# Kernel tuning notes

Hardware: AMD Instinct MI355X
Metric: run time of the kernel (lower is better)

## Reference

```python
import jax, jax.numpy as jnp
import numpy as np

MODEL_DIM = 128
N_ATOMS = 2048
ATOM_SIZE = 512
N_SAMPLES = 2 ** 15
FACTOR = 1.0
TAU = 1.0
B, E = 8, 64


def _stack(x, w0, b0, w1, b1, w2, b2):
    # LinearOutputStack(model_dim, 2, out_channels=...): 2 hidden layers + output
    h = jax.nn.leaky_relu(x @ w0 + b0, 0.2)
    h = jax.nn.leaky_relu(h @ w1 + b1, 0.2)
    return h @ w2 + b2


def _fft_shift(a, shift):
    # a: [B, E, n], shift: [B, E, 1] (fractional shift in units of n samples * 0.5)
    n = a.shape[-1]
    shift_samples = shift * n * 0.5  # [B, E, 1]
    a = jnp.pad(a, ((0, 0), (0, 0), (0, n * 2)))
    spec = jnp.fft.rfft(a, axis=-1, norm='ortho')  # [B, E, n_coeffs] complex
    n_coeffs = spec.shape[-1]
    phase = (jnp.arange(n_coeffs) * 2j * jnp.pi) / n_coeffs  # [n_coeffs]
    spec = spec * jnp.exp(-phase[None, None, :] * shift_samples)
    samples = jnp.fft.irfft(spec, axis=-1, norm='ortho')
    return samples[..., :n]


def setup_inputs() -> dict:
    key = jax.random.key(0)
    ks = jax.random.split(key, 24)
    w = lambda k, i, o: (jax.random.normal(k, (i, o), jnp.float32) * 0.1)
    z = lambda o: jnp.zeros((o,), jnp.float32)
    return {
        'x': jax.random.normal(ks[0], (B, E, MODEL_DIM), jnp.float32),
        'times': jax.random.uniform(ks[1], (B, E, 1), jnp.float32),
        'gumbel_u': jax.random.uniform(ks[2], (B, E, N_ATOMS), jnp.float32),
        'atoms': jax.random.uniform(ks[3], (N_ATOMS, ATOM_SIZE), jnp.float32, -1.0, 1.0),
        'tw0': w(ks[4], MODEL_DIM, MODEL_DIM), 'tb0': z(MODEL_DIM),
        'tw1': w(ks[5], MODEL_DIM, MODEL_DIM), 'tb1': z(MODEL_DIM),
        'tw2': w(ks[6], MODEL_DIM, 1), 'tb2': z(1),
        'sw0': w(ks[7], MODEL_DIM, MODEL_DIM), 'sb0': z(MODEL_DIM),
        'sw1': w(ks[8], MODEL_DIM, MODEL_DIM), 'sb1': z(MODEL_DIM),
        'sw2': w(ks[9], MODEL_DIM, N_ATOMS), 'sb2': z(N_ATOMS),
        'aw0': w(ks[10], MODEL_DIM, MODEL_DIM), 'ab0': z(MODEL_DIM),
        'aw1': w(ks[11], MODEL_DIM, MODEL_DIM), 'ab1': z(MODEL_DIM),
        'aw2': w(ks[12], MODEL_DIM, 1), 'ab2': z(1),
    }


def reference(x, times, gumbel_u, atoms,
              tw0, tb0, tw1, tb1, tw2, tb2,
              sw0, sb0, sw1, sb1, sw2, sb2,
              aw0, ab0, aw1, ab1, aw2, ab2):
    time = jax.nn.sigmoid(_stack(x, tw0, tb0, tw1, tb1, tw2, tb2)) * FACTOR + times  # [B,E,1]
    amp = _stack(x, aw0, ab0, aw1, ab1, aw2, ab2) ** 2  # [B,E,1]
    logits = _stack(x, sw0, sb0, sw1, sb1, sw2, sb2)  # [B,E,N_ATOMS]

    # hard gumbel-softmax with straight-through estimator
    eps = 1e-10
    g = -jnp.log(-jnp.log(gumbel_u + eps) + eps)
    y_soft = jax.nn.softmax((logits + g) / TAU, axis=-1)
    y_hard = jax.nn.one_hot(jnp.argmax(y_soft, axis=-1), N_ATOMS, dtype=y_soft.dtype)
    sel = y_hard - jax.lax.stop_gradient(y_soft) + y_soft

    normed = atoms / (jnp.linalg.norm(atoms, axis=-1, keepdims=True) + 1e-8)
    a = (sel @ normed) * amp  # [B,E,ATOM_SIZE]
    a = jnp.pad(a, ((0, 0), (0, 0), (0, N_SAMPLES - ATOM_SIZE)))  # [B,E,N_SAMPLES]
    final = _fft_shift(a, time)
    return jnp.sum(final, axis=1, keepdims=True)  # [B,1,N_SAMPLES]
```

## Files before the change

kernel.cpp:

```cpp
#include <hip/hip_runtime.h>
#include <math.h>

#define MD 128
#define NA 2048
#define AS 512
#define NS 32768
#define NBE 512
#define W1 768
#define W2 1280
#define PI 3.14159265358979323846
#define KTH ((float)(PI / 98304.0))

__device__ __forceinline__ float lrelu(float v) { return v > 0.f ? v : 0.2f * v; }

__device__ __forceinline__ float p8_far(float tf, float4 A, float4 B, float4 C)
{
  float u  = tf - A.x;
  float th = u * KTH;
  float sn = __sinf(th);
  float cs = __cosf(th);
  float c  = cs * __builtin_amdgcn_rcpf(sn);
  float u2  = __builtin_fmaf(c, c, 1.f);
  float c2  = c + c;
  float u22 = u2 + u2;
  float a2  = c * u2;
  float a3  = (-1.f / 3.f) * __builtin_fmaf(c2, a2, u2 * u2);
  float a4  = 0.5f * __builtin_fmaf(-c, a3, u2 * a2);
  float s5  = __builtin_fmaf(c2, a4, a2 * a2);
  s5        = __builtin_fmaf(-u22, a3, s5);
  float a5  = -0.2f * s5;
  float s6  = __builtin_fmaf(c, a5, a2 * a3);
  s6        = __builtin_fmaf(-u2, a4, s6);
  float a6  = (-1.f / 3.f) * s6;
  float s7  = __builtin_fmaf(c2, a6, a3 * a3);
  s7        = __builtin_fmaf(-u22, a5, s7);
  s7        = __builtin_fmaf(2.f * a2, a4, s7);
  float a7  = (-1.f / 7.f) * s7;
  float s8  = __builtin_fmaf(c, a7, a3 * a4);
  s8        = __builtin_fmaf(-u2, a6, s8);
  s8        = __builtin_fmaf(a2, a5, s8);
  float a8  = -0.25f * s8;
  float y = c * A.w;
  y = __builtin_fmaf(-u2, B.x, y);
  y = __builtin_fmaf(a2, B.y, y);
  y = __builtin_fmaf(a3, B.z, y);
  y = __builtin_fmaf(a4, B.w, y);
  y = __builtin_fmaf(a5, C.x, y);
  y = __builtin_fmaf(a6, C.y, y);
  y = __builtin_fmaf(a7, C.z, y);
  y = __builtin_fmaf(a8, C.w, y);
  bool farq = (tf < A.y) || (tf >= A.z);
  return farq ? y : 0.f;
}

__global__ __launch_bounds__(128) void hidden_kernel(
    const float* __restrict__ x, const float* __restrict__ times,
    const float* __restrict__ tw0, const float* __restrict__ tb0,
    const float* __restrict__ tw1, const float* __restrict__ tb1,
    const float* __restrict__ tw2, const float* __restrict__ tb2,
    const float* __restrict__ sw0, const float* __restrict__ sb0,
    const float* __restrict__ sw1, const float* __restrict__ sb1,
    const float* __restrict__ aw0, const float* __restrict__ ab0,
    const float* __restrict__ aw1, const float* __restrict__ ab1,
    const float* __restrict__ aw2, const float* __restrict__ ab2,
    float* __restrict__ timev, float* __restrict__ ampv,
    float* __restrict__ h2sel, float* __restrict__ out)
{
  const int rg = blockIdx.x;
  const int stack = blockIdx.y;
  const int tid = threadIdx.x;

  {
    const int gtid = (stack * 128 + rg) * 128 + tid;
    float4* out4 = (float4*)out;
    const float4 z = make_float4(0.f, 0.f, 0.f, 0.f);
    for (int i = gtid; i < (8 * NS) / 4; i += 49152) out4[i] = z;
  }

  __shared__ float xs[4][MD];
  __shared__ double dA[4][MD], dB[4][MD];
  __shared__ float fA[4][MD], fB[4][MD];

#pragma unroll
  for (int j = 0; j < 4; ++j) xs[j][tid] = x[(rg * 4 + j) * MD + tid];
  __syncthreads();

  if (stack == 0) {
    {
      double b = (double)tb0[tid];
      double s[4] = {b, b, b, b};
#pragma unroll 8
      for (int k = 0; k < MD; ++k) {
        double w = (double)tw0[k * MD + tid];
#pragma unroll
        for (int j = 0; j < 4; ++j) s[j] += (double)xs[j][k] * w;
      }
#pragma unroll
      for (int j = 0; j < 4; ++j) dA[j][tid] = s[j] > 0.0 ? s[j] : 0.2 * s[j];
      __syncthreads();
    }
    {
      double b = (double)tb1[tid];
      double s[4] = {b, b, b, b};
#pragma unroll 8
      for (int k = 0; k < MD; ++k) {
        double w = (double)tw1[k * MD + tid];
#pragma unroll
        for (int j = 0; j < 4; ++j) s[j] += dA[j][k] * w;
      }
#pragma unroll
      for (int j = 0; j < 4; ++j) dB[j][tid] = s[j] > 0.0 ? s[j] : 0.2 * s[j];
      __syncthreads();
    }
    {
      double w2 = (double)tw2[tid];
#pragma unroll
      for (int j = 0; j < 4; ++j) dA[j][tid] = dB[j][tid] * w2;
      __syncthreads();
      for (int off = 64; off > 0; off >>= 1) {
        if (tid < off) {
#pragma unroll
          for (int j = 0; j < 4; ++j) dA[j][tid] += dA[j][tid + off];
        }
        __syncthreads();
      }
      if (tid == 0) {
#pragma unroll
        for (int j = 0; j < 4; ++j) {
          double tval = dA[j][0] + (double)tb2[0];
          double sg = 1.0 / (1.0 + exp(-tval));
          float tf = (float)sg;
          timev[rg * 4 + j] = tf * 1.0f + times[rg * 4 + j];
        }
      }
    }
  } else if (stack == 1) {
    {
      float b = ab0[tid];
      float s[4] = {b, b, b, b};
#pragma unroll 8
      for (int k = 0; k < MD; ++k) {
        float w = aw0[k * MD + tid];
#pragma unroll
        for (int j = 0; j < 4; ++j) s[j] += xs[j][k] * w;
      }
#pragma unroll
      for (int j = 0; j < 4; ++j) fA[j][tid] = lrelu(s[j]);
      __syncthreads();
    }
    {
      float b = ab1[tid];
      float s[4] = {b, b, b, b};
#pragma unroll 8
      for (int k = 0; k < MD; ++k) {
        float w = aw1[k * MD + tid];
#pragma unroll
        for (int j = 0; j < 4; ++j) s[j] += fA[j][k] * w;
      }
#pragma unroll
      for (int j = 0; j < 4; ++j) fB[j][tid] = lrelu(s[j]);
      __syncthreads();
    }
    {
      float w2 = aw2[tid];
#pragma unroll
      for (int j = 0; j < 4; ++j) fA[j][tid] = fB[j][tid] * w2;
      __syncthreads();
      for (int off = 64; off > 0; off >>= 1) {
        if (tid < off) {
#pragma unroll
          for (int j = 0; j < 4; ++j) fA[j][tid] += fA[j][tid + off];
        }
        __syncthreads();
      }
      if (tid == 0) {
#pragma unroll
        for (int j = 0; j < 4; ++j) {
          float av = fA[j][0] + ab2[0];
          ampv[rg * 4 + j] = av * av;
        }
      }
    }
  } else {
    {
      float b = sb0[tid];
      float s[4] = {b, b, b, b};
#pragma unroll 8
      for (int k = 0; k < MD; ++k) {
        float w = sw0[k * MD + tid];
#pragma unroll
        for (int j = 0; j < 4; ++j) s[j] += xs[j][k] * w;
      }
#pragma unroll
      for (int j = 0; j < 4; ++j) fA[j][tid] = lrelu(s[j]);
      __syncthreads();
    }
    {
      float b = sb1[tid];
      float s[4] = {b, b, b, b};
#pragma unroll 8
      for (int k = 0; k < MD; ++k) {
        float w = sw1[k * MD + tid];
#pragma unroll
        for (int j = 0; j < 4; ++j) s[j] += fA[j][k] * w;
      }
#pragma unroll
      for (int j = 0; j < 4; ++j)
        h2sel[(rg * 4 + j) * MD + tid] = lrelu(s[j]);
    }
  }
}

__global__ __launch_bounds__(128) void logits_kernel(
    const float* __restrict__ h2sel, const float* __restrict__ gu,
    const float* __restrict__ sw2, const float* __restrict__ sb2,
    float2* __restrict__ partials)
{
  const int ot = blockIdx.x;
  const int beg = blockIdx.y;
  const int tid = threadIdx.x;
  const int o = ot * 128 + tid;
  const int wave = tid >> 6, lane = tid & 63;

  __shared__ float h2s[4][MD];
  __shared__ float wv[2][4];
  __shared__ int wi[2][4];

#pragma unroll
  for (int j = 0; j < 4; ++j) h2s[j][tid] = h2sel[(beg * 4 + j) * MD + tid];
  __syncthreads();

  float b = sb2[o];
  float acc[4] = {b, b, b, b};
#pragma unroll 16
  for (int k = 0; k < MD; ++k) {
    float w = sw2[k * NA + o];
#pragma unroll
    for (int j = 0; j < 4; ++j) acc[j] = fmaf(h2s[j][k], w, acc[j]);
  }

#pragma unroll
  for (int j = 0; j < 4; ++j) {
    float u = gu[(beg * 4 + j) * NA + o];
    float g = -logf(-logf(u + 1e-10f) + 1e-10f);
    float v = acc[j] + g;
    int idx = o;
    for (int off = 32; off > 0; off >>= 1) {
      float ov = __shfl_xor(v, off);
      int oi = __shfl_xor(idx, off);
      if (ov > v || (ov == v && oi < idx)) { v = ov; idx = oi; }
    }
    if (lane == 0) { wv[wave][j] = v; wi[wave][j] = idx; }
  }
  __syncthreads();
  if (tid == 0) {
#pragma unroll
    for (int j = 0; j < 4; ++j) {
      float v0 = wv[0][j], v1 = wv[1][j];
      int i0 = wi[0][j], i1 = wi[1][j];
      bool take1 = (v1 > v0) || (v1 == v0 && i1 < i0);
      float bv = take1 ? v1 : v0;
      int bi = take1 ? i1 : i0;
      partials[(beg * 4 + j) * 16 + ot] = make_float2(bv, __int_as_float(bi));
    }
  }
}

__global__ __launch_bounds__(128) void finalize_kernel(
    const float2* __restrict__ partials, const float* __restrict__ timev,
    const float* __restrict__ ampv, const float* __restrict__ atoms,
    float* __restrict__ G, int* __restrict__ m0s, float* __restrict__ fracs,
    float4* __restrict__ params, float4* __restrict__ mom2)
{
  const int be = blockIdx.x;
  const int tid = threadIdx.x;
  __shared__ float red[128];
  __shared__ float m_red[128][13];
  __shared__ float sc_coef, sc_inv;
  __shared__ int sc_idx;

  if (tid < 64) {
    float v = -3.4e38f;
    int idx = 0x7fffffff;
    if (tid < 16) {
      float2 p = partials[be * 16 + tid];
      v = p.x;
      idx = __float_as_int(p.y);
    }
    for (int off = 8; off > 0; off >>= 1) {
      float ov = __shfl_xor(v, off);
      int oi = __shfl_xor(idx, off);
      if (ov > v || (ov == v && oi < idx)) { v = ov; idx = oi; }
    }
    if (tid == 0) sc_idx = idx;
  }
  __syncthreads();
  const int idx = sc_idx;

  const float4 a4 = ((const float4*)(atoms + (size_t)idx * AS))[tid];

  {
    float ss = a4.x * a4.x + a4.y * a4.y + a4.z * a4.z + a4.w * a4.w;
    red[tid] = ss;
    __syncthreads();
    for (int off = 64; off > 0; off >>= 1) {
      if (tid < off) red[tid] += red[tid + off];
      __syncthreads();
    }
    if (tid == 0) {
      sc_inv = 1.f / (sqrtf(red[0]) + 1e-8f);
      double Nc = (double)timev[be] * (1610612736.0 / 49153.0);
      double rr = rint(Nc);
      int m0 = (int)rr;
      float fr = (float)(Nc - rr);
      if (fabsf(fr) < 1e-9f) fr = (fr < 0.f) ? -1e-9f : 1e-9f;
      m0s[be] = m0;
      fracs[be] = fr;
      sc_coef = ampv[be] * ((m0 & 1) ? 1.0f : -1.0f) *
                sinf((float)PI * fr) * (1.0f / 98304.0f);
      red[64] = (float)m0;
      red[65] = fr;
    }
    __syncthreads();
  }

  const float cf = sc_coef * sc_inv;
  float mk[13];
#pragma unroll
  for (int k = 0; k < 13; ++k) mk[k] = 0.f;
  const float av4[4] = {a4.x * cf, a4.y * cf, a4.z * cf, a4.w * cf};
  float4 gv4;
  float* gvp = (float*)&gv4;
  const int t0 = tid * 4;
#pragma unroll
  for (int j = 0; j < 4; ++j) {
    const int t = t0 + j;
    float gv = (j & 1) ? -av4[j] : av4[j];
    gvp[j] = gv;
    float q = (255.5f - (float)t) * KTH;
    float pw = gv;
    mk[0] += pw;
#pragma unroll
    for (int k = 1; k < 13; ++k) { pw *= q; mk[k] += pw; }
  }
  ((float4*)(G + (size_t)be * AS))[tid] = gv4;
#pragma unroll
  for (int k = 0; k < 13; ++k) m_red[tid][k] = mk[k];
  __syncthreads();
  for (int off = 64; off > 0; off >>= 1) {
    if (tid < off) {
#pragma unroll
      for (int k = 0; k < 13; ++k) m_red[tid][k] += m_red[tid + off][k];
    }
    __syncthreads();
  }
  if (tid == 0) {
    int m0 = (int)red[64];
    float fr = red[65];
    float uc = (float)((double)m0 + (double)fr + 255.5);
    params[be * 3 + 0] = make_float4(uc, (float)(m0 - W1), (float)(m0 + W2), m_red[0][0]);
    params[be * 3 + 1] = make_float4(m_red[0][1], m_red[0][2], m_red[0][3], m_red[0][4]);
    params[be * 3 + 2] = make_float4(m_red[0][5], m_red[0][6], m_red[0][7], m_red[0][8]);
    mom2[be] = make_float4(m_red[0][9], m_red[0][10], m_red[0][11], m_red[0][12]);
  }
}

__global__ __launch_bounds__(256) void field_kernel(
    const float4* __restrict__ params, const float4* __restrict__ mom2,
    const float* __restrict__ G, const int* __restrict__ m0s,
    const float* __restrict__ fracs, float* __restrict__ out)
{
  __shared__ float4 SMEM[768];
  const int bid = blockIdx.x;
  const int tid = threadIdx.x;

  if (bid >= 512) {
    const int idx2 = bid - 512;
    const int b = idx2 >> 7;
    const int seg = idx2 & 127;
    float* Cf   = (float*)SMEM;
    int*   scnt = (int*)(Cf + 32);
    int*   slst = scnt + 2;

    const int w = tid >> 6;
    const int e = tid & 63;
    if (w < 2) {
      const int tile = 2 * seg + w;
      const int be = b * 64 + e;
      const float4 A  = params[be * 3 + 0];
      const float4 B4 = params[be * 3 + 1];
      const float4 C4 = params[be * 3 + 2];
      const float4 D4 = mom2[be];
      const float M[13] = {A.w, B4.x, B4.y, B4.z, B4.w,
                           C4.x, C4.y, C4.z, C4.w, D4.x, D4.y, D4.z, D4.w};

      const float ts = (float)(tile * 128);
      const float te = ts + 128.f;
      const float lo = A.y, hi = A.z;
      const bool inter   = (lo < te) && (hi > ts);
      const bool inside  = (lo <= ts) && (te <= hi);
      const bool special = inter && !inside;

      float Bj[13];
#pragma unroll
      for (int j = 0; j < 13; ++j) Bj[j] = 0.f;

      if (!inter) {
        const float th = (ts + 63.5f - A.x) * KTH;
        const float sn = __sinf(th), cs = __cosf(th);
        const float c = cs * __builtin_amdgcn_rcpf(sn);
        float a[13];
        a[0] = c; a[1] = -__builtin_fmaf(c, c, 1.f);
        float s;
        s = 2.f * a[0] * a[1];                                      a[2]  = -0.5f * s;
        s = __builtin_fmaf(2.f * a[0], a[2], a[1] * a[1]);          a[3]  = (-1.f / 3.f) * s;
        s = 2.f * (a[0] * a[3] + a[1] * a[2]);                      a[4]  = -0.25f * s;
        s = __builtin_fmaf(2.f, a[0] * a[4] + a[1] * a[3], a[2] * a[2]); a[5] = -0.2f * s;
        s = 2.f * (a[0] * a[5] + a[1] * a[4] + a[2] * a[3]);        a[6]  = (-1.f / 6.f) * s;
        s = __builtin_fmaf(2.f, a[0] * a[6] + a[1] * a[5] + a[2] * a[4], a[3] * a[3]); a[7] = (-1.f / 7.f) * s;
        s = 2.f * (a[0] * a[7] + a[1] * a[6] + a[2] * a[5] + a[3] * a[4]); a[8] = -0.125f * s;
        s = __builtin_fmaf(2.f, a[0] * a[8] + a[1] * a[7] + a[2] * a[6] + a[3] * a[5], a[4] * a[4]); a[9] = (-1.f / 9.f) * s;
        s = 2.f * (a[0] * a[9] + a[1] * a[8] + a[2] * a[7] + a[3] * a[6] + a[4] * a[5]); a[10] = -0.1f * s;
        s = __builtin_fmaf(2.f, a[0] * a[10] + a[1] * a[9] + a[2] * a[8] + a[3] * a[7] + a[4] * a[6], a[5] * a[5]); a[11] = (-1.f / 11.f) * s;
        s = 2.f * (a[0] * a[11] + a[1] * a[10] + a[2] * a[9] + a[3] * a[8] + a[4] * a[7] + a[5] * a[6]); a[12] = (-1.f / 12.f) * s;

        const float BIN[13][13] = {
          {1,0,0,0,0,0,0,0,0,0,0,0,0},
          {1,1,0,0,0,0,0,0,0,0,0,0,0},
          {1,2,1,0,0,0,0,0,0,0,0,0,0},
          {1,3,3,1,0,0,0,0,0,0,0,0,0},
          {1,4,6,4,1,0,0,0,0,0,0,0,0},
          {1,5,10,10,5,1,0,0,0,0,0,0,0},
          {1,6,15,20,15,6,1,0,0,0,0,0,0},
          {1,7,21,35,35,21,7,1,0,0,0,0,0},
          {1,8,28,56,70,56,28,8,1,0,0,0,0},
          {1,9,36,84,126,126,84,36,9,1,0,0,0},
          {1,10,45,120,210,252,210,120,45,10,1,0,0},
          {1,11,55,165,330,462,462,330,165,55,11,1,0},
          {1,12,66,220,495,792,924,792,495,220,66,12,1}};
#pragma unroll
        for (int j = 0; j < 13; ++j) {
          float acc = 0.f;
#pragma unroll
          for (int m = j; m < 13; ++m)
            acc = __builtin_fmaf(BIN[m][j] * a[m], M[m - j], acc);
          Bj[j] = acc;
        }
      }

#pragma unroll
      for (int j = 0; j < 13; ++j) {
#pragma unroll
        for (int off = 32; off > 0; off >>= 1)
          Bj[j] += __shfl_xor(Bj[j], off);
      }
      if (e == 0) {
#pragma unroll
        for (int j = 0; j < 13; ++j) Cf[w * 16 + j] = Bj[j];
      }
      unsigned long long msk = __ballot(special);
      if (special) {
        int pos = __popcll(msk & ((1ull << e) - 1ull));
        slst[w * 64 + pos] = be;
      }
      if (e == 0) scnt[w] = (int)__popcll(msk);
    }
    __syncthreads();

    const int t = seg * 256 + tid;
    const int tw = tid >> 7;
    const float* cc = Cf + tw * 16;
    const float tf = (float)t;
    const float h = (tf - ((float)((2 * seg + tw) * 128) + 63.5f)) * KTH;
    float y = cc[12];
    y = __builtin_fmaf(y, h, cc[11]);
    y = __builtin_fmaf(y, h, cc[10]);
    y = __builtin_fmaf(y, h, cc[9]);
    y = __builtin_fmaf(y, h, cc[8]);
    y = __builtin_fmaf(y, h, cc[7]);
    y = __builtin_fmaf(y, h, cc[6]);
    y = __builtin_fmaf(y, h, cc[5]);
    y = __builtin_fmaf(y, h, cc[4]);
    y = __builtin_fmaf(y, h, cc[3]);
    y = __builtin_fmaf(y, h, cc[2]);
    y = __builtin_fmaf(y, h, cc[1]);
    y = __builtin_fmaf(y, h, cc[0]);

    const int cnt = scnt[tw];
    for (int i = 0; i < cnt; ++i) {
      const int se = slst[tw * 64 + i];
      const float4 A  = params[se * 3 + 0];
      const float4 B4 = params[se * 3 + 1];
      const float4 C4 = params[se * 3 + 2];
      y += p8_far(tf, A, B4, C4);
    }
    atomicAdd(&out[b * NS + t], (t & 1) ? -y : y);
    return;
  }

  const int be = bid;
  const int m0 = m0s[be];
  const int start = m0 - W1;
  if (start >= NS) return;
  const float fr = fracs[be];
  const int b = be >> 6;

  float4* Tsplit = SMEM;
  float*  Tf = (float*)Tsplit;
  float*  Gl = (float*)(SMEM + 640);
  const float4* Gl4 = SMEM + 640;

  for (int i = tid; i < AS; i += 256) Gl[i] = G[be * AS + i];
  for (int i = tid; i < 2560; i += 256) {
    int v = start - 511 + i;
    float w = (float)(v - m0) - fr;
    float th = w * KTH;
    float q = th * th;
    float sn = th * __builtin_fmaf(q, __builtin_fmaf(q, (1.f / 120.f), (-1.f / 6.f)), 1.f);
    float cs = __builtin_fmaf(q, __builtin_fmaf(q, (1.f / 24.f), -0.5f), 1.f);
    float val = cs * __builtin_amdgcn_rcpf(sn);
    int g = i >> 2;
    int s = (g >> 1) * 4 + (i & 3) + (g & 1) * 1280;
    Tf[s] = val;
  }
  __syncthreads();

  float acc[8];
#pragma unroll
  for (int r = 0; r < 8; ++r) acc[r] = 0.f;

  float Wf[16];
  {
    float4 qa = Tsplit[tid];
    float4 qb = Tsplit[320 + tid];
    Wf[0] = qa.x; Wf[1] = qa.y; Wf[2] = qa.z; Wf[3] = qa.w;
    Wf[4] = qb.x; Wf[5] = qb.y; Wf[6] = qb.z; Wf[7] = qb.w;
  }
#pragma unroll 4
  for (int k = 0; k < 64; ++k) {
    float4 qa = Tsplit[tid + k + 1];
    float4 qb = Tsplit[320 + tid + k + 1];
    Wf[8]  = qa.x; Wf[9]  = qa.y; Wf[10] = qa.z; Wf[11] = qa.w;
    Wf[12] = qb.x; Wf[13] = qb.y; Wf[14] = qb.z; Wf[15] = qb.w;
    const int tc = 504 - 8 * k;
    const float4 gq0 = Gl4[tc >> 2];
    const float4 gq1 = Gl4[(tc >> 2) + 1];
    const float gvals[8] = {gq0.x, gq0.y, gq0.z, gq0.w,
                            gq1.x, gq1.y, gq1.z, gq1.w};
#pragma unroll
    for (int d = 0; d < 8; ++d) {
      const float gv = gvals[d];
#pragma unroll
      for (int r = 0; r < 8; ++r)
        acc[r] = fmaf(gv, Wf[7 + r - d], acc[r]);
    }
#pragma unroll
    for (int m = 0; m < 8; ++m) Wf[m] = Wf[m + 8];
  }

  const int tb = start + tid * 8;
#pragma unroll
  for (int r = 0; r < 8; ++r) {
    int t = tb + r;
    if (t >= 0 && t < NS) {
      float v = (t & 1) ? -acc[r] : acc[r];
      atomicAdd(&out[b * NS + t], v);
    }
  }
}

extern "C" void kernel_launch(void* const* d_in, const int* in_sizes, int n_in,
                              void* d_out, int out_size, void* d_ws, size_t ws_size,
                              hipStream_t stream) {
  const float* x     = (const float*)d_in[0];
  const float* times = (const float*)d_in[1];
  const float* gu    = (const float*)d_in[2];
  const float* atoms = (const float*)d_in[3];
  const float* tw0 = (const float*)d_in[4];  const float* tb0 = (const float*)d_in[5];
  const float* tw1 = (const float*)d_in[6];  const float* tb1 = (const float*)d_in[7];
  const float* tw2 = (const float*)d_in[8];  const float* tb2 = (const float*)d_in[9];
  const float* sw0 = (const float*)d_in[10]; const float* sb0 = (const float*)d_in[11];
  const float* sw1 = (const float*)d_in[12]; const float* sb1 = (const float*)d_in[13];
  const float* sw2 = (const float*)d_in[14]; const float* sb2 = (const float*)d_in[15];
  const float* aw0 = (const float*)d_in[16]; const float* ab0 = (const float*)d_in[17];
  const float* aw1 = (const float*)d_in[18]; const float* ab1 = (const float*)d_in[19];
  const float* aw2 = (const float*)d_in[20]; const float* ab2 = (const float*)d_in[21];

  char* wsb = (char*)d_ws;
  float*  G        = (float*)wsb;
  int*    m0s      = (int*)(wsb + 1048576);
  float*  fracs    = (float*)(wsb + 1050624);
  float4* params   = (float4*)(wsb + 1052672);
  float*  timev    = (float*)(wsb + 1077248);
  float*  ampv     = (float*)(wsb + 1079296);
  float4* mom2     = (float4*)(wsb + 1081344);
  float*  h2sel    = (float*)(wsb + 1089536);
  float2* partials = (float2*)(wsb + 1351680);

  hidden_kernel<<<dim3(NBE / 4, 3), 128, 0, stream>>>(
      x, times, tw0, tb0, tw1, tb1, tw2, tb2,
      sw0, sb0, sw1, sb1, aw0, ab0, aw1, ab1, aw2, ab2,
      timev, ampv, h2sel, (float*)d_out);

  logits_kernel<<<dim3(16, NBE / 4), 128, 0, stream>>>(h2sel, gu, sw2, sb2, partials);

  finalize_kernel<<<NBE, 128, 0, stream>>>(partials, timev, ampv, atoms,
                                           G, m0s, fracs, params, mom2);

  field_kernel<<<1536, 256, 0, stream>>>(params, mom2, G, m0s, fracs,
                                         (float*)d_out);
}
```

Measured before the change: 69.27 us.

## Fuse hidden and logits kernels, recomputing selection MLP per output tile

Merges the hidden-layer kernel and the logits/argmax kernel into one launch of 2304 blocks. The first 2048 blocks each recompute the two selection-stack hidden layers for their four rows before computing a 128-wide logits tile and the gumbel argmax, which removes the h2sel round trip and one kernel launch. The remaining blocks compute the time and amp stacks, and the output zeroing is spread one float4 per thread. The cost is recomputing the 128x128 hidden layers 16 times per row group.

Result: slower. 72.60 us (+4.8%).

```diff
diff --git a/kernel.cpp b/kernel.cpp
--- a/kernel.cpp
+++ b/kernel.cpp
@@ -53,33 +53,113 @@
   return farq ? y : 0.f;
 }
 
-__global__ __launch_bounds__(128) void hidden_kernel(
+__global__ __launch_bounds__(128) void prepA_kernel(
     const float* __restrict__ x, const float* __restrict__ times,
+    const float* __restrict__ gu,
     const float* __restrict__ tw0, const float* __restrict__ tb0,
     const float* __restrict__ tw1, const float* __restrict__ tb1,
     const float* __restrict__ tw2, const float* __restrict__ tb2,
     const float* __restrict__ sw0, const float* __restrict__ sb0,
     const float* __restrict__ sw1, const float* __restrict__ sb1,
+    const float* __restrict__ sw2, const float* __restrict__ sb2,
     const float* __restrict__ aw0, const float* __restrict__ ab0,
     const float* __restrict__ aw1, const float* __restrict__ ab1,
     const float* __restrict__ aw2, const float* __restrict__ ab2,
     float* __restrict__ timev, float* __restrict__ ampv,
-    float* __restrict__ h2sel, float* __restrict__ out)
+    float2* __restrict__ partials, float* __restrict__ out)
 {
-  const int rg = blockIdx.x;
-  const int stack = blockIdx.y;
+  const int bid = blockIdx.x;
   const int tid = threadIdx.x;
 
   {
-    const int gtid = (stack * 128 + rg) * 128 + tid;
-    float4* out4 = (float4*)out;
-    const float4 z = make_float4(0.f, 0.f, 0.f, 0.f);
-    for (int i = gtid; i < (8 * NS) / 4; i += 49152) out4[i] = z;
+    const int gtid = bid * 128 + tid;
+    if (gtid < (8 * NS) / 4) {
+      ((float4*)out)[gtid] = make_float4(0.f, 0.f, 0.f, 0.f);
+    }
   }
 
   __shared__ float xs[4][MD];
+  __shared__ float fA[4][MD], fB[4][MD];
+
+  if (bid < 2048) {
+    const int ot  = bid & 15;
+    const int beg = bid >> 4;
+    const int o = ot * 128 + tid;
+    const int wave = tid >> 6, lane = tid & 63;
+    __shared__ float wv[2][4];
+    __shared__ int wi[2][4];
+
+#pragma unroll
+    for (int j = 0; j < 4; ++j) xs[j][tid] = x[(beg * 4 + j) * MD + tid];
+    __syncthreads();
+
+    {
+      float b = sb0[tid];
+      float s[4] = {b, b, b, b};
+#pragma unroll 8
+      for (int k = 0; k < MD; ++k) {
+        float w = sw0[k * MD + tid];
+#pragma unroll
+        for (int j = 0; j < 4; ++j) s[j] += xs[j][k] * w;
+      }
+#pragma unroll
+      for (int j = 0; j < 4; ++j) fA[j][tid] = lrelu(s[j]);
+      __syncthreads();
+    }
+    {
+      float b = sb1[tid];
+      float s[4] = {b, b, b, b};
+#pragma unroll 8
+      for (int k = 0; k < MD; ++k) {
+        float w = sw1[k * MD + tid];
+#pragma unroll
+        for (int j = 0; j < 4; ++j) s[j] += fA[j][k] * w;
+      }
+#pragma unroll
+      for (int j = 0; j < 4; ++j) fB[j][tid] = lrelu(s[j]);
+      __syncthreads();
+    }
+
+    float b = sb2[o];
+    float acc[4] = {b, b, b, b};
+#pragma unroll 16
+    for (int k = 0; k < MD; ++k) {
+      float w = sw2[k * NA + o];
+#pragma unroll
+      for (int j = 0; j < 4; ++j) acc[j] = fmaf(fB[j][k], w, acc[j]);
+    }
+
+#pragma unroll
+    for (int j = 0; j < 4; ++j) {
+      float u = gu[(beg * 4 + j) * NA + o];
+      float g = -logf(-logf(u + 1e-10f) + 1e-10f);
+      float v = acc[j] + g;
+      int idx = o;
+      for (int off = 32; off > 0; off >>= 1) {
+        float ov = __shfl_xor(v, off);
+        int oi = __shfl_xor(idx, off);
+        if (ov > v || (ov == v && oi < idx)) { v = ov; idx = oi; }
+      }
+      if (lane == 0) { wv[wave][j] = v; wi[wave][j] = idx; }
+    }
+    __syncthreads();
+    if (tid == 0) {
+#pragma unroll
+      for (int j = 0; j < 4; ++j) {
+        float v0 = wv[0][j], v1 = wv[1][j];
+        int i0 = wi[0][j], i1 = wi[1][j];
+        bool take1 = (v1 > v0) || (v1 == v0 && i1 < i0);
+        float bv = take1 ? v1 : v0;
+        int bi = take1 ? i1 : i0;
+        partials[(beg * 4 + j) * 16 + ot] = make_float2(bv, __int_as_float(bi));
+      }
+    }
+    return;
+  }
+
   __shared__ double dA[4][MD], dB[4][MD];
-  __shared__ float fA[4][MD], fB[4][MD];
+  const int stack = (bid < 2176) ? 0 : 1;
+  const int rg = bid - (stack == 0 ? 2048 : 2176);
 
 #pragma unroll
   for (int j = 0; j < 4; ++j) xs[j][tid] = x[(rg * 4 + j) * MD + tid];
@@ -134,7 +214,7 @@
         }
       }
     }
-  } else if (stack == 1) {
+  } else {
     {
       float b = ab0[tid];
       float s[4] = {b, b, b, b};
@@ -180,88 +260,6 @@
           ampv[rg * 4 + j] = av * av;
         }
       }
-    }
-  } else {
-    {
-      float b = sb0[tid];
-      float s[4] = {b, b, b, b};
-#pragma unroll 8
-      for (int k = 0; k < MD; ++k) {
-        float w = sw0[k * MD + tid];
-#pragma unroll
-        for (int j = 0; j < 4; ++j) s[j] += xs[j][k] * w;
-      }
-#pragma unroll
-      for (int j = 0; j < 4; ++j) fA[j][tid] = lrelu(s[j]);
-      __syncthreads();
-    }
-    {
-      float b = sb1[tid];
-      float s[4] = {b, b, b, b};
-#pragma unroll 8
-      for (int k = 0; k < MD; ++k) {
-        float w = sw1[k * MD + tid];
-#pragma unroll
-        for (int j = 0; j < 4; ++j) s[j] += fA[j][k] * w;
-      }
-#pragma unroll
-      for (int j = 0; j < 4; ++j)
-        h2sel[(rg * 4 + j) * MD + tid] = lrelu(s[j]);
-    }
-  }
-}
-
-__global__ __launch_bounds__(128) void logits_kernel(
-    const float* __restrict__ h2sel, const float* __restrict__ gu,
-    const float* __restrict__ sw2, const float* __restrict__ sb2,
-    float2* __restrict__ partials)
-{
-  const int ot = blockIdx.x;
-  const int beg = blockIdx.y;
-  const int tid = threadIdx.x;
-  const int o = ot * 128 + tid;
-  const int wave = tid >> 6, lane = tid & 63;
-
-  __shared__ float h2s[4][MD];
-  __shared__ float wv[2][4];
-  __shared__ int wi[2][4];
-
-#pragma unroll
-  for (int j = 0; j < 4; ++j) h2s[j][tid] = h2sel[(beg * 4 + j) * MD + tid];
-  __syncthreads();
-
-  float b = sb2[o];
-  float acc[4] = {b, b, b, b};
-#pragma unroll 16
-  for (int k = 0; k < MD; ++k) {
-    float w = sw2[k * NA + o];
-#pragma unroll
-    for (int j = 0; j < 4; ++j) acc[j] = fmaf(h2s[j][k], w, acc[j]);
-  }
-
-#pragma unroll
-  for (int j = 0; j < 4; ++j) {
-    float u = gu[(beg * 4 + j) * NA + o];
-    float g = -logf(-logf(u + 1e-10f) + 1e-10f);
-    float v = acc[j] + g;
-    int idx = o;
-    for (int off = 32; off > 0; off >>= 1) {
-      float ov = __shfl_xor(v, off);
-      int oi = __shfl_xor(idx, off);
-      if (ov > v || (ov == v && oi < idx)) { v = ov; idx = oi; }
-    }
-    if (lane == 0) { wv[wave][j] = v; wi[wave][j] = idx; }
-  }
-  __syncthreads();
-  if (tid == 0) {
-#pragma unroll
-    for (int j = 0; j < 4; ++j) {
-      float v0 = wv[0][j], v1 = wv[1][j];
-      int i0 = wi[0][j], i1 = wi[1][j];
-      bool take1 = (v1 > v0) || (v1 == v0 && i1 < i0);
-      float bv = take1 ? v1 : v0;
-      int bi = take1 ? i1 : i0;
-      partials[(beg * 4 + j) * 16 + ot] = make_float2(bv, __int_as_float(bi));
     }
   }
 }
@@ -594,15 +592,13 @@
   float*  timev    = (float*)(wsb + 1077248);
   float*  ampv     = (float*)(wsb + 1079296);
   float4* mom2     = (float4*)(wsb + 1081344);
-  float*  h2sel    = (float*)(wsb + 1089536);
-  float2* partials = (float2*)(wsb + 1351680);
-
-  hidden_kernel<<<dim3(NBE / 4, 3), 128, 0, stream>>>(
-      x, times, tw0, tb0, tw1, tb1, tw2, tb2,
-      sw0, sb0, sw1, sb1, aw0, ab0, aw1, ab1, aw2, ab2,
-      timev, ampv, h2sel, (float*)d_out);
-
-  logits_kernel<<<dim3(16, NBE / 4), 128, 0, stream>>>(h2sel, gu, sw2, sb2, partials);
+  float2* partials = (float2*)(wsb + 1089536);
+
+  prepA_kernel<<<2304, 128, 0, stream>>>(
+      x, times, gu, tw0, tb0, tw1, tb1, tw2, tb2,
+      sw0, sb0, sw1, sb1, sw2, sb2,
+      aw0, ab0, aw1, ab1, aw2, ab2,
+      timev, ampv, partials, (float*)d_out);
 
   finalize_kernel<<<NBE, 128, 0, stream>>>(partials, timev, ampv, atoms,
                                            G, m0s, fracs, params, mom2);
```
